# Kernel optimization log

Measured on AMD Instinct MI355X. Metric: run time of the kernel, lower is better.

## Reference

```python
import jax, jax.numpy as jnp
import numpy as np

B, S, D, H, F, E = 8, 1024, 1024, 16, 3584, 2
HD = D // H
NUM_LABELS = 2
EPS = 1e-6


def setup_inputs() -> dict:
    key = jax.random.key(0)
    ks = jax.random.split(key, 10)
    w = lambda k, shape: jax.random.normal(k, shape, jnp.float32) * 0.02
    return {
        "hidden_states": jax.random.normal(ks[0], (B, S, D), jnp.float32),
        "ln1_w": jnp.ones((D,), jnp.float32),
        "q_w": w(ks[1], (D, D)),
        "k_w": w(ks[2], (D, D)),
        "v_w": w(ks[3], (D, D)),
        "o_w": w(ks[4], (D, D)),
        "ln2_w": jnp.ones((D,), jnp.float32),
        "router_w": w(ks[5], (D, E)),
        "gate_w": w(ks[6], (E, D, F)),
        "up_w": w(ks[7], (E, D, F)),
        "down_w": w(ks[8], (E, F, D)),
        "final_ln_w": jnp.ones((D,), jnp.float32),
        "score_w": w(ks[9], (D, NUM_LABELS)),
    }


def rmsnorm(x, w):
    var = jnp.mean(jnp.square(x), axis=-1, keepdims=True)
    return x * jax.lax.rsqrt(var + EPS) * w


def reference(hidden_states, ln1_w, q_w, k_w, v_w, o_w, ln2_w, router_w,
              gate_w, up_w, down_w, final_ln_w, score_w):
    x = hidden_states  # [B,S,D]
    # --- attention block (Jamba attention: no RoPE, no bias, causal) ---
    res = x
    h = rmsnorm(x, ln1_w)
    q = (h @ q_w).reshape(B, S, H, HD).transpose(0, 2, 1, 3)  # [B,H,S,HD]
    k = (h @ k_w).reshape(B, S, H, HD).transpose(0, 2, 1, 3)
    v = (h @ v_w).reshape(B, S, H, HD).transpose(0, 2, 1, 3)
    scores = jnp.einsum("bhqd,bhkd->bhqk", q, k) / np.sqrt(HD).astype(np.float32)
    causal = jnp.tril(jnp.ones((S, S), bool))
    scores = jnp.where(causal, scores, jnp.finfo(jnp.float32).min)
    attn = jax.nn.softmax(scores, axis=-1)
    ctx = jnp.einsum("bhqk,bhkd->bhqd", attn, v)
    attn_out = ctx.transpose(0, 2, 1, 3).reshape(B, S, D) @ o_w
    x = res + attn_out
    # --- top-1 MoE FFN (Jamba: softmax router, top-k, NO renormalization) ---
    res = x
    h = rmsnorm(x, ln2_w).reshape(B * S, D)
    router_logits = h @ router_w  # [N,E]
    probs = jax.nn.softmax(router_logits.astype(jnp.float32), axis=-1)
    top_w = jnp.max(probs, axis=-1)       # top-1 weight
    sel = jnp.argmax(probs, axis=-1)      # selected expert id
    moe = jnp.zeros_like(h)
    for e in range(E):  # fixed tiny loop over experts
        y = (jax.nn.silu(h @ gate_w[e]) * (h @ up_w[e])) @ down_w[e]
        moe = moe + jnp.where(sel == e, top_w, 0.0)[:, None] * y
    x = res + moe.reshape(B, S, D)
    # --- final RMSNorm + score head on first token ---
    x = rmsnorm(x, final_ln_w)
    logits = x[:, 0, :] @ score_w  # [B, NUM_LABELS]
    return logits
```

## Files before the change

kernel.cpp:

```cpp
#include <hip/hip_runtime.h>
#include <math.h>

#define B 8
#define S 1024
#define D 1024
#define F 3584

#define KSV 64
#define CHV 16
#define KS5 32
#define CH5 32
#define KS6 224
#define CH6 16

#define LD4(p) (*(const float4*)(p))
typedef float f4v __attribute__((ext_vector_type(4)));
#define NTLD(p) __builtin_nontemporal_load((const f4v*)(p))

#define FMA4(A, s, W) { (A).x += (s)*(W).x; (A).y += (s)*(W).y; (A).z += (s)*(W).z; (A).w += (s)*(W).w; }

#define BB8(bb, ACC, XS, CH, koff) { \
  float4 xa = LD4((XS) + (bb)*(CH) + (koff)); \
  float4 xb = LD4((XS) + (bb)*(CH) + (koff) + 4); \
  FMA4(ACC, xa.x, w0); FMA4(ACC, xa.y, w1); FMA4(ACC, xa.z, w2); FMA4(ACC, xa.w, w3); \
  FMA4(ACC, xb.x, w4); FMA4(ACC, xb.y, w5); FMA4(ACC, xb.z, w6); FMA4(ACC, xb.w, w7); }

#define ALL8(XS, CH, koff) \
  BB8(0, acc0, XS, CH, koff) BB8(1, acc1, XS, CH, koff) \
  BB8(2, acc2, XS, CH, koff) BB8(3, acc3, XS, CH, koff) \
  BB8(4, acc4, XS, CH, koff) BB8(5, acc5, XS, CH, koff) \
  BB8(6, acc6, XS, CH, koff) BB8(7, acc7, XS, CH, koff)

__device__ __forceinline__ float block_sum256(float v, volatile float* buf) {
  #pragma unroll
  for (int o = 32; o; o >>= 1) v += __shfl_down(v, o);
  __syncthreads();
  if ((threadIdx.x & 63) == 0) buf[threadIdx.x >> 6] = v;
  __syncthreads();
  return buf[0] + buf[1] + buf[2] + buf[3];
}

__device__ __forceinline__ void mv16(const float* __restrict__ W, int j,
                                     float* __restrict__ Pout,
                                     const float* xs,
                                     const int* ssel, int e) {
  const float4* Wp = (const float4*)(W + j);
  const int st = D / 4;
  float4 acc0 = {0,0,0,0}, acc1 = {0,0,0,0}, acc2 = {0,0,0,0}, acc3 = {0,0,0,0};
  float4 acc4 = {0,0,0,0}, acc5 = {0,0,0,0}, acc6 = {0,0,0,0}, acc7 = {0,0,0,0};
  f4v w0 = NTLD(Wp+0*st), w1 = NTLD(Wp+1*st), w2 = NTLD(Wp+2*st), w3 = NTLD(Wp+3*st);
  f4v w4 = NTLD(Wp+4*st), w5 = NTLD(Wp+5*st), w6 = NTLD(Wp+6*st), w7 = NTLD(Wp+7*st);
  f4v v0 = NTLD(Wp+8*st), v1 = NTLD(Wp+9*st), v2 = NTLD(Wp+10*st), v3 = NTLD(Wp+11*st);
  f4v v4 = NTLD(Wp+12*st), v5 = NTLD(Wp+13*st), v6 = NTLD(Wp+14*st), v7 = NTLD(Wp+15*st);
  ALL8(xs, CHV, 0);
  w0 = v0; w1 = v1; w2 = v2; w3 = v3; w4 = v4; w5 = v5; w6 = v6; w7 = v7;
  ALL8(xs, CHV, 8);
  #define MV_ST(bb, ACC) \
    if (!ssel || ssel[bb] == e) *(float4*)(Pout + (bb)*(size_t)D + j) = ACC;
  MV_ST(0, acc0) MV_ST(1, acc1) MV_ST(2, acc2) MV_ST(3, acc3)
  MV_ST(4, acc4) MV_ST(5, acc5) MV_ST(6, acc6) MV_ST(7, acc7)
  #undef MV_ST
}

__global__ __launch_bounds__(256, 2) void k_mvp_v(const float* __restrict__ hs,
                                                  const float* __restrict__ ln1w,
                                                  const float* __restrict__ vw,
                                                  float* __restrict__ Vp) {
  __shared__ float xs[8 * CHV];
  __shared__ float scsh[8];
  int tid = threadIdx.x;
  int w = tid >> 6, lane = tid & 63;
  #pragma unroll
  for (int b2 = 0; b2 < 2; b2++) {
    int b = w * 2 + b2;
    const float4* hp = (const float4*)(hs + (size_t)b * S * D);
    float ss = 0.f;
    #pragma unroll
    for (int t = 0; t < 4; t++) {
      float4 v = hp[lane * 4 + t];
      ss += v.x*v.x + v.y*v.y + v.z*v.z + v.w*v.w;
    }
    #pragma unroll
    for (int o = 32; o; o >>= 1) ss += __shfl_down(ss, o);
    if (lane == 0) scsh[b] = rsqrtf(ss * (1.f / (float)D) + 1e-6f);
  }
  __syncthreads();
  int i0 = blockIdx.x * CHV;
  if (tid < 128) {
    int bb = tid >> 4, ii = tid & 15;
    xs[tid] = hs[(size_t)bb * S * D + i0 + ii] * scsh[bb] * ln1w[i0 + ii];
  }
  __syncthreads();
  mv16(vw + (size_t)i0 * D, tid * 4, Vp + (size_t)blockIdx.x * 8 * D, xs, 0, 0);
}

__global__ __launch_bounds__(256, 2) void k_ored(const float* __restrict__ Vp,
                                                 const float* __restrict__ ow,
                                                 float* __restrict__ Op) {
  __shared__ float xs[8 * CHV];
  int tid = threadIdx.x;
  int i0 = blockIdx.x * CHV;
  if (tid < 128) {
    int bb = tid >> 4, ii = tid & 15;
    float s = 0.f;
    #pragma unroll 16
    for (int p = 0; p < KSV; p++) s += Vp[((size_t)p * 8 + bb) * D + i0 + ii];
    xs[bb * CHV + ii] = s;
  }
  __syncthreads();
  mv16(ow + (size_t)i0 * D, tid * 4, Op + (size_t)blockIdx.x * 8 * D, xs, 0, 0);
}

__global__ void k_mid(const float* __restrict__ hs, const float* __restrict__ Op,
                      const float* __restrict__ ln2, const float* __restrict__ rw,
                      float* __restrict__ xr, float* __restrict__ h2,
                      float* __restrict__ topw, int* __restrict__ sel) {
  __shared__ float buf[4];
  int b = blockIdx.x;
  int idx = threadIdx.x * 4;
  float4 x = LD4(hs + (size_t)b * S * D + idx);
  #pragma unroll 16
  for (int p = 0; p < KSV; p++) {
    float4 v = LD4(Op + ((size_t)p * 8 + b) * D + idx);
    x.x += v.x; x.y += v.y; x.z += v.z; x.w += v.w;
  }
  *(float4*)(xr + b * D + idx) = x;
  float ss = x.x*x.x + x.y*x.y + x.z*x.z + x.w*x.w;
  float tot = block_sum256(ss, buf);
  float sc = rsqrtf(tot * (1.f / (float)D) + 1e-6f);
  float4 wv = LD4(ln2 + idx);
  float4 h;
  h.x = x.x*sc*wv.x; h.y = x.y*sc*wv.y; h.z = x.z*sc*wv.z; h.w = x.w*sc*wv.w;
  *(float4*)(h2 + b * D + idx) = h;
  float r0 = h.x * rw[idx * 2]     + h.y * rw[(idx + 1) * 2] +
             h.z * rw[(idx + 2) * 2] + h.w * rw[(idx + 3) * 2];
  float r1 = h.x * rw[idx * 2 + 1]     + h.y * rw[(idx + 1) * 2 + 1] +
             h.z * rw[(idx + 2) * 2 + 1] + h.w * rw[(idx + 3) * 2 + 1];
  r0 = block_sum256(r0, buf);
  r1 = block_sum256(r1, buf);
  if (threadIdx.x == 0) {
    float m = fmaxf(r0, r1);
    float e0 = __expf(r0 - m), e1 = __expf(r1 - m);
    float inv = 1.f / (e0 + e1);
    float p0 = e0 * inv, p1 = e1 * inv;
    topw[b] = fmaxf(p0, p1);
    sel[b] = (p1 > p0) ? 1 : 0;
  }
}

__global__ __launch_bounds__(256, 2) void k_gateup(const float* __restrict__ h2,
                                                   const float* __restrict__ gw,
                                                   const float* __restrict__ uw,
                                                   const int* __restrict__ sel,
                                                   float* __restrict__ Pgu) {
  __shared__ float xs[8 * CH5];
  __shared__ int ssel[8];
  int tid = threadIdx.x;
  int kc = blockIdx.y, colt = blockIdx.x;
  int i0 = kc * CH5;
  { int bb = tid >> 5, r = tid & 31;
    xs[tid] = h2[bb * D + i0 + r]; }
  if (tid < 8) ssel[tid] = sel[tid];
  __syncthreads();
  int c = colt * 1024 + tid * 4;
  int m = c / F;
  int j = c - m * F;
  const float* base = (m < 2 ? gw : uw) + (size_t)(m & 1) * D * F;
  const float4* Wp = (const float4*)(base + (size_t)i0 * F + j);
  const int st = F / 4;
  float4 acc0 = {0,0,0,0}, acc1 = {0,0,0,0}, acc2 = {0,0,0,0}, acc3 = {0,0,0,0};
  float4 acc4 = {0,0,0,0}, acc5 = {0,0,0,0}, acc6 = {0,0,0,0}, acc7 = {0,0,0,0};
  f4v w0 = NTLD(Wp+0*st), w1 = NTLD(Wp+1*st), w2 = NTLD(Wp+2*st), w3 = NTLD(Wp+3*st);
  f4v w4 = NTLD(Wp+4*st), w5 = NTLD(Wp+5*st), w6 = NTLD(Wp+6*st), w7 = NTLD(Wp+7*st);
  Wp += 8 * st;
  #pragma unroll
  for (int t = 0; t < CH5 / 8 - 1; t++) {
    f4v n0 = NTLD(Wp+0*st), n1 = NTLD(Wp+1*st), n2 = NTLD(Wp+2*st), n3 = NTLD(Wp+3*st);
    f4v n4 = NTLD(Wp+4*st), n5 = NTLD(Wp+5*st), n6 = NTLD(Wp+6*st), n7 = NTLD(Wp+7*st);
    Wp += 8 * st;
    ALL8(xs, CH5, t * 8);
    w0 = n0; w1 = n1; w2 = n2; w3 = n3; w4 = n4; w5 = n5; w6 = n6; w7 = n7;
  }
  ALL8(xs, CH5, CH5 - 8);
  int me = m & 1;
  #define GU_ST(bb, ACC) \
    if (ssel[bb] == me) \
      *(float4*)(Pgu + (((size_t)kc * 4 + m) * 8 + (bb)) * F + j) = ACC;
  GU_ST(0, acc0) GU_ST(1, acc1) GU_ST(2, acc2) GU_ST(3, acc3)
  GU_ST(4, acc4) GU_ST(5, acc5) GU_ST(6, acc6) GU_ST(7, acc7)
  #undef GU_ST
}

__global__ __launch_bounds__(256, 2) void k_down(const float* __restrict__ Pgu,
                                                 const float* __restrict__ dw,
                                                 const int* __restrict__ sel,
                                                 float* __restrict__ Dp) {
  __shared__ float xs[8 * CH6];
  __shared__ int ssel[8];
  int tid = threadIdx.x;
  int e = blockIdx.x & 1, ch = blockIdx.x >> 1, i0 = ch * CH6;
  if (tid < 8) ssel[tid] = sel[tid];
  __syncthreads();
  if (tid < 128) {
    int bb = tid >> 4, ii = tid & 15;
    float r = 0.f;
    if (ssel[bb] == e) {
      float ga = 0.f, ua = 0.f;
      #pragma unroll
      for (int kc = 0; kc < KS5; kc++) {
        ga += Pgu[(((size_t)kc * 4 + e)     * 8 + bb) * F + i0 + ii];
        ua += Pgu[(((size_t)kc * 4 + 2 + e) * 8 + bb) * F + i0 + ii];
      }
      r = (ga / (1.f + __expf(-ga))) * ua;
    }
    xs[bb * CH6 + ii] = r;
  }
  __syncthreads();
  mv16(dw + (size_t)e * F * D + (size_t)i0 * D, tid * 4,
       Dp + (((size_t)ch * 2 + e) * 8) * D, xs, ssel, e);
}

__global__ void k_final(const float* __restrict__ xr, const float* __restrict__ Dp,
                        const float* __restrict__ topw, const int* __restrict__ sel,
                        const float* __restrict__ flw, const float* __restrict__ sw,
                        float* __restrict__ out) {
  __shared__ float buf[4];
  int b = blockIdx.x;
  int e = sel[b];
  float tw = topw[b];
  int idx = threadIdx.x * 4;
  float4 y = {0,0,0,0};
  #pragma unroll 16
  for (int p = 0; p < KS6; p++) {
    float4 v = LD4(Dp + (((size_t)p * 2 + e) * 8 + b) * D + idx);
    y.x += v.x; y.y += v.y; y.z += v.z; y.w += v.w;
  }
  float4 x = LD4(xr + b * D + idx);
  x.x += tw * y.x; x.y += tw * y.y; x.z += tw * y.z; x.w += tw * y.w;
  float ss = x.x*x.x + x.y*x.y + x.z*x.z + x.w*x.w;
  float tot = block_sum256(ss, buf);
  float sc = rsqrtf(tot * (1.f / (float)D) + 1e-6f);
  float4 wv = LD4(flw + idx);
  float n0 = x.x*sc*wv.x, n1 = x.y*sc*wv.y, n2 = x.z*sc*wv.z, n3 = x.w*sc*wv.w;
  float l0 = n0 * sw[idx * 2]     + n1 * sw[(idx + 1) * 2] +
             n2 * sw[(idx + 2) * 2] + n3 * sw[(idx + 3) * 2];
  float l1 = n0 * sw[idx * 2 + 1]     + n1 * sw[(idx + 1) * 2 + 1] +
             n2 * sw[(idx + 2) * 2 + 1] + n3 * sw[(idx + 3) * 2 + 1];
  l0 = block_sum256(l0, buf);
  l1 = block_sum256(l1, buf);
  if (threadIdx.x == 0) { out[b * 2 + 0] = l0; out[b * 2 + 1] = l1; }
}

extern "C" void kernel_launch(void* const* d_in, const int* in_sizes, int n_in,
                              void* d_out, int out_size, void* d_ws, size_t ws_size,
                              hipStream_t stream) {
  const float* hs  = (const float*)d_in[0];
  const float* ln1 = (const float*)d_in[1];
  const float* vw  = (const float*)d_in[4];
  const float* ow  = (const float*)d_in[5];
  const float* ln2 = (const float*)d_in[6];
  const float* rw  = (const float*)d_in[7];
  const float* gw  = (const float*)d_in[8];
  const float* uw  = (const float*)d_in[9];
  const float* dw  = (const float*)d_in[10];
  const float* flw = (const float*)d_in[11];
  const float* sw  = (const float*)d_in[12];

  float* ws = (float*)d_ws;
  float* Vp   = ws;
  float* Op   = ws + 524288;
  float* xr   = ws + 1048576;
  float* h2   = ws + 1056768;
  float* tw8  = ws + 1064960;
  int*   sel8 = (int*)(ws + 1064968);
  float* Pgu  = ws + 1064992;
  float* Dp   = ws + 4735008;

  k_mvp_v<<<KSV, 256, 0, stream>>>(hs, ln1, vw, Vp);
  k_ored<<<KSV, 256, 0, stream>>>(Vp, ow, Op);
  k_mid<<<8, 256, 0, stream>>>(hs, Op, ln2, rw, xr, h2, tw8, sel8);
  k_gateup<<<dim3(14, KS5), 256, 0, stream>>>(h2, gw, uw, sel8, Pgu);
  k_down<<<2 * KS6, 256, 0, stream>>>(Pgu, dw, sel8, Dp);
  k_final<<<8, 256, 0, stream>>>(xr, Dp, tw8, sel8, flw, sw, (float*)d_out);
}
```

Baseline: 220.9 us.

## Prefetch MoE expert weights into LLC using idle blocks of early kernels

The small attention-phase kernels are launched with extra blocks that stream the gate, up and down expert weights (about 29MB each) through the cache hierarchy so that the later gate/up and down matvecs can hit the MI355X last-level cache instead of HBM. Weight loads in k_gateup and k_down switch from nontemporal to normal loads so the prefetched lines can be reused. This overlaps weight fetch with the latency-bound attention and router kernels. The risk is that the weights (about 86MB in total) may not all stay resident in the LLC, that the prefetch blocks compete for bandwidth with the real work, and that a dummy write is needed to keep the loads from being removed.

```diff
diff --git a/kernel.cpp b/kernel.cpp
--- a/kernel.cpp
+++ b/kernel.cpp
@@ -13,15 +13,14 @@
 #define KS6 224
 #define CH6 16
 
-#define LD4(p) (*(const float4*)(p))
 typedef float f4v __attribute__((ext_vector_type(4)));
-#define NTLD(p) __builtin_nontemporal_load((const f4v*)(p))
+#define LD4(p) (*(const f4v*)(p))
 
 #define FMA4(A, s, W) { (A).x += (s)*(W).x; (A).y += (s)*(W).y; (A).z += (s)*(W).z; (A).w += (s)*(W).w; }
 
 #define BB8(bb, ACC, XS, CH, koff) { \
-  float4 xa = LD4((XS) + (bb)*(CH) + (koff)); \
-  float4 xb = LD4((XS) + (bb)*(CH) + (koff) + 4); \
+  f4v xa = LD4((XS) + (bb)*(CH) + (koff)); \
+  f4v xb = LD4((XS) + (bb)*(CH) + (koff) + 4); \
   FMA4(ACC, xa.x, w0); FMA4(ACC, xa.y, w1); FMA4(ACC, xa.z, w2); FMA4(ACC, xa.w, w3); \
   FMA4(ACC, xb.x, w4); FMA4(ACC, xb.y, w5); FMA4(ACC, xb.z, w6); FMA4(ACC, xb.w, w7); }
 
@@ -40,44 +39,71 @@
   return buf[0] + buf[1] + buf[2] + buf[3];
 }
 
+template<int NT>
+__device__ __forceinline__ f4v wld(const f4v* p) {
+  if constexpr (NT) return __builtin_nontemporal_load(p);
+  else return *p;
+}
+
+__device__ __forceinline__ void prefetch_llc(const float* __restrict__ w,
+                                             int nf4, int pid, int nblk,
+                                             int tid, float* __restrict__ dummy) {
+  const f4v* p = (const f4v*)w;
+  int stride = nblk * 256;
+  f4v acc = {0.f, 0.f, 0.f, 0.f};
+  for (int i = pid * 256 + tid; i < nf4; i += stride) acc += p[i];
+  float t = acc.x + acc.y + acc.z + acc.w;
+  if (t > 1e30f) dummy[0] = t;
+}
+
+template<int NT>
 __device__ __forceinline__ void mv16(const float* __restrict__ W, int j,
                                      float* __restrict__ Pout,
                                      const float* xs,
                                      const int* ssel, int e) {
-  const float4* Wp = (const float4*)(W + j);
+  const f4v* Wp = (const f4v*)(W + j);
   const int st = D / 4;
-  float4 acc0 = {0,0,0,0}, acc1 = {0,0,0,0}, acc2 = {0,0,0,0}, acc3 = {0,0,0,0};
-  float4 acc4 = {0,0,0,0}, acc5 = {0,0,0,0}, acc6 = {0,0,0,0}, acc7 = {0,0,0,0};
-  f4v w0 = NTLD(Wp+0*st), w1 = NTLD(Wp+1*st), w2 = NTLD(Wp+2*st), w3 = NTLD(Wp+3*st);
-  f4v w4 = NTLD(Wp+4*st), w5 = NTLD(Wp+5*st), w6 = NTLD(Wp+6*st), w7 = NTLD(Wp+7*st);
-  f4v v0 = NTLD(Wp+8*st), v1 = NTLD(Wp+9*st), v2 = NTLD(Wp+10*st), v3 = NTLD(Wp+11*st);
-  f4v v4 = NTLD(Wp+12*st), v5 = NTLD(Wp+13*st), v6 = NTLD(Wp+14*st), v7 = NTLD(Wp+15*st);
+  f4v acc0 = {0,0,0,0}, acc1 = {0,0,0,0}, acc2 = {0,0,0,0}, acc3 = {0,0,0,0};
+  f4v acc4 = {0,0,0,0}, acc5 = {0,0,0,0}, acc6 = {0,0,0,0}, acc7 = {0,0,0,0};
+  f4v w0 = wld<NT>(Wp+0*st), w1 = wld<NT>(Wp+1*st), w2 = wld<NT>(Wp+2*st), w3 = wld<NT>(Wp+3*st);
+  f4v w4 = wld<NT>(Wp+4*st), w5 = wld<NT>(Wp+5*st), w6 = wld<NT>(Wp+6*st), w7 = wld<NT>(Wp+7*st);
+  f4v v0 = wld<NT>(Wp+8*st), v1 = wld<NT>(Wp+9*st), v2 = wld<NT>(Wp+10*st), v3 = wld<NT>(Wp+11*st);
+  f4v v4 = wld<NT>(Wp+12*st), v5 = wld<NT>(Wp+13*st), v6 = wld<NT>(Wp+14*st), v7 = wld<NT>(Wp+15*st);
   ALL8(xs, CHV, 0);
   w0 = v0; w1 = v1; w2 = v2; w3 = v3; w4 = v4; w5 = v5; w6 = v6; w7 = v7;
   ALL8(xs, CHV, 8);
   #define MV_ST(bb, ACC) \
-    if (!ssel || ssel[bb] == e) *(float4*)(Pout + (bb)*(size_t)D + j) = ACC;
+    if (!ssel || ssel[bb] == e) *(f4v*)(Pout + (bb)*(size_t)D + j) = ACC;
   MV_ST(0, acc0) MV_ST(1, acc1) MV_ST(2, acc2) MV_ST(3, acc3)
   MV_ST(4, acc4) MV_ST(5, acc5) MV_ST(6, acc6) MV_ST(7, acc7)
   #undef MV_ST
 }
 
+#define NF4_GATE (2 * D * F / 4)
+
 __global__ __launch_bounds__(256, 2) void k_mvp_v(const float* __restrict__ hs,
                                                   const float* __restrict__ ln1w,
                                                   const float* __restrict__ vw,
-                                                  float* __restrict__ Vp) {
+                                                  const float* __restrict__ gw,
+                                                  float* __restrict__ Vp,
+                                                  float* __restrict__ dummy) {
   __shared__ float xs[8 * CHV];
   __shared__ float scsh[8];
   int tid = threadIdx.x;
+  int bid = blockIdx.x;
+  if (bid >= KSV) {
+    prefetch_llc(gw, NF4_GATE, bid - KSV, 256 - KSV, tid, dummy);
+    return;
+  }
   int w = tid >> 6, lane = tid & 63;
   #pragma unroll
   for (int b2 = 0; b2 < 2; b2++) {
     int b = w * 2 + b2;
-    const float4* hp = (const float4*)(hs + (size_t)b * S * D);
+    const f4v* hp = (const f4v*)(hs + (size_t)b * S * D);
     float ss = 0.f;
     #pragma unroll
     for (int t = 0; t < 4; t++) {
-      float4 v = hp[lane * 4 + t];
+      f4v v = hp[lane * 4 + t];
       ss += v.x*v.x + v.y*v.y + v.z*v.z + v.w*v.w;
     }
     #pragma unroll
@@ -85,21 +111,28 @@
     if (lane == 0) scsh[b] = rsqrtf(ss * (1.f / (float)D) + 1e-6f);
   }
   __syncthreads();
-  int i0 = blockIdx.x * CHV;
+  int i0 = bid * CHV;
   if (tid < 128) {
     int bb = tid >> 4, ii = tid & 15;
     xs[tid] = hs[(size_t)bb * S * D + i0 + ii] * scsh[bb] * ln1w[i0 + ii];
   }
   __syncthreads();
-  mv16(vw + (size_t)i0 * D, tid * 4, Vp + (size_t)blockIdx.x * 8 * D, xs, 0, 0);
+  mv16<1>(vw + (size_t)i0 * D, tid * 4, Vp + (size_t)bid * 8 * D, xs, 0, 0);
 }
 
 __global__ __launch_bounds__(256, 2) void k_ored(const float* __restrict__ Vp,
                                                  const float* __restrict__ ow,
-                                                 float* __restrict__ Op) {
+                                                 const float* __restrict__ uw,
+                                                 float* __restrict__ Op,
+                                                 float* __restrict__ dummy) {
   __shared__ float xs[8 * CHV];
   int tid = threadIdx.x;
-  int i0 = blockIdx.x * CHV;
+  int bid = blockIdx.x;
+  if (bid >= KSV) {
+    prefetch_llc(uw, NF4_GATE, bid - KSV, 256 - KSV, tid, dummy);
+    return;
+  }
+  int i0 = bid * CHV;
   if (tid < 128) {
     int bb = tid >> 4, ii = tid & 15;
     float s = 0.f;
@@ -108,30 +141,36 @@
     xs[bb * CHV + ii] = s;
   }
   __syncthreads();
-  mv16(ow + (size_t)i0 * D, tid * 4, Op + (size_t)blockIdx.x * 8 * D, xs, 0, 0);
+  mv16<1>(ow + (size_t)i0 * D, tid * 4, Op + (size_t)bid * 8 * D, xs, 0, 0);
 }
 
 __global__ void k_mid(const float* __restrict__ hs, const float* __restrict__ Op,
                       const float* __restrict__ ln2, const float* __restrict__ rw,
+                      const float* __restrict__ dwp,
                       float* __restrict__ xr, float* __restrict__ h2,
-                      float* __restrict__ topw, int* __restrict__ sel) {
+                      float* __restrict__ topw, int* __restrict__ sel,
+                      float* __restrict__ dummy) {
   __shared__ float buf[4];
   int b = blockIdx.x;
+  if (b >= 8) {
+    prefetch_llc(dwp, NF4_GATE, b - 8, 248, threadIdx.x, dummy);
+    return;
+  }
   int idx = threadIdx.x * 4;
-  float4 x = LD4(hs + (size_t)b * S * D + idx);
+  f4v x = LD4(hs + (size_t)b * S * D + idx);
   #pragma unroll 16
   for (int p = 0; p < KSV; p++) {
-    float4 v = LD4(Op + ((size_t)p * 8 + b) * D + idx);
+    f4v v = LD4(Op + ((size_t)p * 8 + b) * D + idx);
     x.x += v.x; x.y += v.y; x.z += v.z; x.w += v.w;
   }
-  *(float4*)(xr + b * D + idx) = x;
+  *(f4v*)(xr + b * D + idx) = x;
   float ss = x.x*x.x + x.y*x.y + x.z*x.z + x.w*x.w;
   float tot = block_sum256(ss, buf);
   float sc = rsqrtf(tot * (1.f / (float)D) + 1e-6f);
-  float4 wv = LD4(ln2 + idx);
-  float4 h;
+  f4v wv = LD4(ln2 + idx);
+  f4v h;
   h.x = x.x*sc*wv.x; h.y = x.y*sc*wv.y; h.z = x.z*sc*wv.z; h.w = x.w*sc*wv.w;
-  *(float4*)(h2 + b * D + idx) = h;
+  *(f4v*)(h2 + b * D + idx) = h;
   float r0 = h.x * rw[idx * 2]     + h.y * rw[(idx + 1) * 2] +
              h.z * rw[(idx + 2) * 2] + h.w * rw[(idx + 3) * 2];
   float r1 = h.x * rw[idx * 2 + 1]     + h.y * rw[(idx + 1) * 2 + 1] +
@@ -166,17 +205,17 @@
   int m = c / F;
   int j = c - m * F;
   const float* base = (m < 2 ? gw : uw) + (size_t)(m & 1) * D * F;
-  const float4* Wp = (const float4*)(base + (size_t)i0 * F + j);
+  const f4v* Wp = (const f4v*)(base + (size_t)i0 * F + j);
   const int st = F / 4;
-  float4 acc0 = {0,0,0,0}, acc1 = {0,0,0,0}, acc2 = {0,0,0,0}, acc3 = {0,0,0,0};
-  float4 acc4 = {0,0,0,0}, acc5 = {0,0,0,0}, acc6 = {0,0,0,0}, acc7 = {0,0,0,0};
-  f4v w0 = NTLD(Wp+0*st), w1 = NTLD(Wp+1*st), w2 = NTLD(Wp+2*st), w3 = NTLD(Wp+3*st);
-  f4v w4 = NTLD(Wp+4*st), w5 = NTLD(Wp+5*st), w6 = NTLD(Wp+6*st), w7 = NTLD(Wp+7*st);
+  f4v acc0 = {0,0,0,0}, acc1 = {0,0,0,0}, acc2 = {0,0,0,0}, acc3 = {0,0,0,0};
+  f4v acc4 = {0,0,0,0}, acc5 = {0,0,0,0}, acc6 = {0,0,0,0}, acc7 = {0,0,0,0};
+  f4v w0 = Wp[0*st], w1 = Wp[1*st], w2 = Wp[2*st], w3 = Wp[3*st];
+  f4v w4 = Wp[4*st], w5 = Wp[5*st], w6 = Wp[6*st], w7 = Wp[7*st];
   Wp += 8 * st;
   #pragma unroll
   for (int t = 0; t < CH5 / 8 - 1; t++) {
-    f4v n0 = NTLD(Wp+0*st), n1 = NTLD(Wp+1*st), n2 = NTLD(Wp+2*st), n3 = NTLD(Wp+3*st);
-    f4v n4 = NTLD(Wp+4*st), n5 = NTLD(Wp+5*st), n6 = NTLD(Wp+6*st), n7 = NTLD(Wp+7*st);
+    f4v n0 = Wp[0*st], n1 = Wp[1*st], n2 = Wp[2*st], n3 = Wp[3*st];
+    f4v n4 = Wp[4*st], n5 = Wp[5*st], n6 = Wp[6*st], n7 = Wp[7*st];
     Wp += 8 * st;
     ALL8(xs, CH5, t * 8);
     w0 = n0; w1 = n1; w2 = n2; w3 = n3; w4 = n4; w5 = n5; w6 = n6; w7 = n7;
@@ -185,7 +224,7 @@
   int me = m & 1;
   #define GU_ST(bb, ACC) \
     if (ssel[bb] == me) \
-      *(float4*)(Pgu + (((size_t)kc * 4 + m) * 8 + (bb)) * F + j) = ACC;
+      *(f4v*)(Pgu + (((size_t)kc * 4 + m) * 8 + (bb)) * F + j) = ACC;
   GU_ST(0, acc0) GU_ST(1, acc1) GU_ST(2, acc2) GU_ST(3, acc3)
   GU_ST(4, acc4) GU_ST(5, acc5) GU_ST(6, acc6) GU_ST(7, acc7)
   #undef GU_ST
@@ -216,8 +255,8 @@
     xs[bb * CH6 + ii] = r;
   }
   __syncthreads();
-  mv16(dw + (size_t)e * F * D + (size_t)i0 * D, tid * 4,
-       Dp + (((size_t)ch * 2 + e) * 8) * D, xs, ssel, e);
+  mv16<0>(dw + (size_t)e * F * D + (size_t)i0 * D, tid * 4,
+          Dp + (((size_t)ch * 2 + e) * 8) * D, xs, ssel, e);
 }
 
 __global__ void k_final(const float* __restrict__ xr, const float* __restrict__ Dp,
@@ -229,18 +268,18 @@
   int e = sel[b];
   float tw = topw[b];
   int idx = threadIdx.x * 4;
-  float4 y = {0,0,0,0};
+  f4v y = {0,0,0,0};
   #pragma unroll 16
   for (int p = 0; p < KS6; p++) {
-    float4 v = LD4(Dp + (((size_t)p * 2 + e) * 8 + b) * D + idx);
+    f4v v = LD4(Dp + (((size_t)p * 2 + e) * 8 + b) * D + idx);
     y.x += v.x; y.y += v.y; y.z += v.z; y.w += v.w;
   }
-  float4 x = LD4(xr + b * D + idx);
+  f4v x = LD4(xr + b * D + idx);
   x.x += tw * y.x; x.y += tw * y.y; x.z += tw * y.z; x.w += tw * y.w;
   float ss = x.x*x.x + x.y*x.y + x.z*x.z + x.w*x.w;
   float tot = block_sum256(ss, buf);
   float sc = rsqrtf(tot * (1.f / (float)D) + 1e-6f);
-  float4 wv = LD4(flw + idx);
+  f4v wv = LD4(flw + idx);
   float n0 = x.x*sc*wv.x, n1 = x.y*sc*wv.y, n2 = x.z*sc*wv.z, n3 = x.w*sc*wv.w;
   float l0 = n0 * sw[idx * 2]     + n1 * sw[(idx + 1) * 2] +
              n2 * sw[(idx + 2) * 2] + n3 * sw[(idx + 3) * 2];
@@ -275,10 +314,11 @@
   int*   sel8 = (int*)(ws + 1064968);
   float* Pgu  = ws + 1064992;
   float* Dp   = ws + 4735008;
-
-  k_mvp_v<<<KSV, 256, 0, stream>>>(hs, ln1, vw, Vp);
-  k_ored<<<KSV, 256, 0, stream>>>(Vp, ow, Op);
-  k_mid<<<8, 256, 0, stream>>>(hs, Op, ln2, rw, xr, h2, tw8, sel8);
+  float* dummy = ws + 8405024;
+
+  k_mvp_v<<<256, 256, 0, stream>>>(hs, ln1, vw, gw, Vp, dummy);
+  k_ored<<<256, 256, 0, stream>>>(Vp, ow, uw, Op, dummy);
+  k_mid<<<256, 256, 0, stream>>>(hs, Op, ln2, rw, dw, xr, h2, tw8, sel8, dummy);
   k_gateup<<<dim3(14, KS5), 256, 0, stream>>>(h2, gw, uw, sel8, Pgu);
   k_down<<<2 * KS6, 256, 0, stream>>>(Pgu, dw, sel8, Dp);
   k_final<<<8, 256, 0, stream>>>(xr, Dp, tw8, sel8, flw, sw, (float*)d_out);
```

Measured after the change: 244.7 us. 10.8% more time.
